# Kernel optimization log

Hardware: AMD Instinct MI355X
Metric: run time of the kernel (lower is better)

The kernel has to match this reference:

```python
import jax, jax.numpy as jnp
import numpy as np

N, E, F_IN, HID, HEADS, OUT_DIM, G = 50000, 600000, 92, 32, 8, 1, 512
EPS = 1e-5


def setup_inputs() -> dict:
    key = jax.random.key(0)
    ks = jax.random.split(key, 30)
    s = 0.1
    d1 = HID * HEADS  # 256
    inp = {
        "x": jax.random.normal(ks[0], (N, F_IN), dtype=jnp.float32),
        "edge_index": jax.random.randint(ks[1], (2, E), 0, N),
        "edge_attr": jax.random.uniform(ks[2], (E, 1), dtype=jnp.float32),
        "batch": jnp.sort(jax.random.randint(ks[3], (N,), 0, G)),
        # conv1 (heads=8, concat)
        "W1": jax.random.normal(ks[4], (F_IN, d1)) * s,
        "We1": jax.random.normal(ks[5], (1, d1)) * s,
        "as1": jax.random.normal(ks[6], (HEADS, HID)) * s,
        "ad1": jax.random.normal(ks[7], (HEADS, HID)) * s,
        "ae1": jax.random.normal(ks[8], (HEADS, HID)) * s,
        "b1": jax.random.normal(ks[9], (d1,)) * s,
        # bn1 (eval mode, running stats)
        "g1": jnp.ones((d1,)), "be1": jnp.zeros((d1,)),
        "m1": jax.random.normal(ks[10], (d1,)) * s, "v1": jnp.ones((d1,)),
        # conv2 (heads=1)
        "W2": jax.random.normal(ks[11], (d1, HID)) * s,
        "We2": jax.random.normal(ks[12], (1, HID)) * s,
        "as2": jax.random.normal(ks[13], (1, HID)) * s,
        "ad2": jax.random.normal(ks[14], (1, HID)) * s,
        "ae2": jax.random.normal(ks[15], (1, HID)) * s,
        "b2": jax.random.normal(ks[16], (HID,)) * s,
        # bn2
        "g2": jnp.ones((HID,)), "be2": jnp.zeros((HID,)),
        "m2": jax.random.normal(ks[17], (HID,)) * s, "v2": jnp.ones((HID,)),
        # final fc
        "fcW": jax.random.normal(ks[18], (HID, OUT_DIM)) * s,
        "fcb": jnp.zeros((OUT_DIM,)),
    }
    return inp


def _gat_conv(x, edge_index, edge_attr, W, We, a_s, a_d, a_e, b, heads, ch):
    """PyG GATConv with edge_dim, add_self_loops=True (fill_value='mean'), concat."""
    n = x.shape[0]
    src, dst = edge_index[0], edge_index[1]
    # self loops: loop edge_attr = mean of incoming edge_attr per node
    cnt = jax.ops.segment_sum(jnp.ones((edge_attr.shape[0],), edge_attr.dtype), dst, n)
    loop_attr = jax.ops.segment_sum(edge_attr, dst, n) / jnp.clip(cnt, 1.0)[:, None]
    ar = jnp.arange(n)
    src = jnp.concatenate([src, ar])
    dst = jnp.concatenate([dst, ar])
    ea = jnp.concatenate([edge_attr, loop_attr], axis=0)
    h = (x @ W).reshape(n, heads, ch)                 # [N,H,C]
    al_s = jnp.sum(h * a_s, axis=-1)                  # [N,H]
    al_d = jnp.sum(h * a_d, axis=-1)                  # [N,H]
    he = (ea @ We).reshape(-1, heads, ch)             # [E',H,C]
    al_e = jnp.sum(he * a_e, axis=-1)                 # [E',H]
    alpha = jax.nn.leaky_relu(al_s[src] + al_d[dst] + al_e, 0.2)
    # scatter softmax over destination segments
    mx = jax.ops.segment_max(alpha, dst, n)
    w = jnp.exp(alpha - mx[dst])
    den = jax.ops.segment_sum(w, dst, n)
    w = w / den[dst]                                  # [E',H]
    out = jax.ops.segment_sum(h[src] * w[:, :, None], dst, n)  # [N,H,C]
    return out.reshape(n, heads * ch) + b


def _bn_eval(x, g, b, m, v):
    return (x - m) * (g / jnp.sqrt(v + EPS)) + b


def reference(x, edge_index, edge_attr, batch,
              W1, We1, as1, ad1, ae1, b1, g1, be1, m1, v1,
              W2, We2, as2, ad2, ae2, b2, g2, be2, m2, v2,
              fcW, fcb):
    h = _gat_conv(x, edge_index, edge_attr, W1, We1, as1, ad1, ae1, b1, HEADS, HID)
    h = jax.nn.relu(_bn_eval(h, g1, be1, m1, v1))
    # dropout is identity in eval mode
    h = _gat_conv(h, edge_index, edge_attr, W2, We2, as2, ad2, ae2, b2, 1, HID)
    h = jax.nn.relu(_bn_eval(h, g2, be2, m2, v2))
    # global mean pool over graphs
    sums = jax.ops.segment_sum(h, batch, G)
    cnt = jax.ops.segment_sum(jnp.ones((h.shape[0],), h.dtype), batch, G)
    pooled = sums / jnp.clip(cnt, 1.0)[:, None]
    return pooled @ fcW + fcb
```

## Files before the change

kernel.cpp:

```cpp
#include <hip/hip_runtime.h>
#include <hip/hip_bf16.h>

#define N_NODES 50000
#define N_EDGES 600000
#define F_IN    92
#define KPAD    96
#define HID     32
#define HEADS   8
#define D1      256
#define HS_LD   264
#define G_GRAPHS 512
#define EPSV    1e-5f
#define NCHUNK  49
#define DEGBLK  2344

using short8  = __attribute__((ext_vector_type(8))) short;
using f32x4   = __attribute__((ext_vector_type(4))) float;
using f32x2   = __attribute__((ext_vector_type(2))) float;

__device__ __forceinline__ float bf2f(unsigned short u) {
    return __uint_as_float(((unsigned)u) << 16);
}
__device__ __forceinline__ unsigned short f2bf(float f) {
    unsigned u = __float_as_uint(f);
    return (unsigned short)((u + 0x7FFFu + ((u >> 16) & 1u)) >> 16);
}


__global__ __launch_bounds__(256) void k_deg_setup(
        const int* __restrict__ ei, int* __restrict__ deg,
        const float* __restrict__ W1, const float* __restrict__ W2,
        const float* __restrict__ We1, const float* __restrict__ ae1,
        const float* __restrict__ We2, const float* __restrict__ ae2,
        const float* __restrict__ as1, const float* __restrict__ ad1,
        const float* __restrict__ b1, const float* __restrict__ g1,
        const float* __restrict__ be1, const float* __restrict__ m1,
        const float* __restrict__ v1,
        const float* __restrict__ b2, const float* __restrict__ g2,
        const float* __restrict__ be2, const float* __restrict__ m2,
        const float* __restrict__ v2,
        unsigned short* __restrict__ W1p, unsigned short* __restrict__ W2p,
        float* __restrict__ va, float* __restrict__ wedot,
        float* __restrict__ bnA1, float* __restrict__ bnB1,
        float* __restrict__ bnA2, float* __restrict__ bnB2) {
    int blk = blockIdx.x, t = threadIdx.x;
    if (blk < DEGBLK) {
        int e = blk * 256 + t;
        if (e < N_EDGES) atomicAdd(&deg[ei[N_EDGES + e]], 1);
        return;
    }
    int b = blk - DEGBLK;
    if (b < 96) {
        int gid = b * 256 + t;
        int k = gid >> 8, col = gid & 255;
        unsigned short v = 0;
        if (k < F_IN) v = f2bf(W1[k * D1 + col]);
        W1p[(((k >> 3) * D1) + col) * 8 + (k & 7)] = v;
    } else if (b < 128) {
        int gid = (b - 96) * 256 + t;
        int k = gid >> 5, col = gid & 31;
        W2p[(((k >> 3) * 32) + col) * 8 + (k & 7)] = f2bf(W2[gid]);
    } else if (b < 134) {
        int gid = (b - 128) * 256 + t;
        if (gid < 2 * HEADS * F_IN) {
            int which = gid / (HEADS * F_IN), rem = gid % (HEADS * F_IN);
            int h = rem / F_IN, k = rem % F_IN;
            const float* av = which ? ad1 : as1;
            float s = 0.f;
            #pragma unroll 8
            for (int c = 0; c < HID; ++c) s += W1[k * D1 + h * HID + c] * av[h * HID + c];
            va[gid] = s;
        }
    } else if (b == 134) {
        if (t < HEADS) {
            float a = 0.f;
            for (int c = 0; c < HID; ++c) a += We1[t * HID + c] * ae1[t * HID + c];
            wedot[t] = a;
        } else if (t == HEADS) {
            float a = 0.f;
            for (int c = 0; c < HID; ++c) a += We2[c] * ae2[c];
            wedot[HEADS] = a;
        }
    } else {
        if (t < D1) {
            float sc = g1[t] * __frsqrt_rn(v1[t] + EPSV);
            bnA1[t] = sc;
            bnB1[t] = (b1[t] - m1[t]) * sc + be1[t];
        }
        if (t < HID) {
            float sc = g2[t] * __frsqrt_rn(v2[t] + EPSV);
            bnA2[t] = sc;
            bnB2[t] = (b2[t] - m2[t]) * sc + be2[t];
        }
    }
}

__global__ void k_partial(const int* __restrict__ deg, int* __restrict__ partials) {
    int b = blockIdx.x;
    int s = 0;
    for (int j = 0; j < 4; ++j) {
        int i = b * 1024 + j * 256 + threadIdx.x;
        if (i < N_NODES) s += deg[i];
    }
    for (int off = 32; off; off >>= 1) s += __shfl_down(s, off, 64);
    __shared__ int sm[4];
    if ((threadIdx.x & 63) == 0) sm[threadIdx.x >> 6] = s;
    __syncthreads();
    if (threadIdx.x == 0) partials[b] = sm[0] + sm[1] + sm[2] + sm[3];
}

__global__ void k_scanc(const int* __restrict__ deg, const int* __restrict__ partials,
                        int* __restrict__ row_off, int* __restrict__ cursor) {
    int b = blockIdx.x;
    int t = threadIdx.x;
    __shared__ int smp;
    if (t < 64) {
        int pv = (t < b) ? partials[t] : 0;
        #pragma unroll
        for (int off = 32; off; off >>= 1) pv += __shfl_down(pv, off, 64);
        if (t == 0) smp = pv;
    }
    int base_i = b * 1024 + t * 4;
    int v[4]; int s = 0;
    #pragma unroll
    for (int j = 0; j < 4; ++j) {
        int i = base_i + j;
        v[j] = (i < N_NODES) ? deg[i] : 0;
        s += v[j];
    }
    __shared__ int sm[256];
    sm[t] = s;
    __syncthreads();
    int val = s;
    for (int off = 1; off < 256; off <<= 1) {
        int add = (t >= off) ? sm[t - off] : 0;
        __syncthreads();
        val += add;
        sm[t] = val;
        __syncthreads();
    }
    int base = smp + (val - s);
    #pragma unroll
    for (int j = 0; j < 4; ++j) {
        int i = base_i + j;
        if (i < N_NODES) { row_off[i] = base; cursor[i] = base; }
        base += v[j];
    }
}

__global__ void k_fill(const int* __restrict__ ei, const float* __restrict__ ea,
                       int* __restrict__ cursor, int2* __restrict__ adj) {
    int e = blockIdx.x * 256 + threadIdx.x;
    if (e < N_EDGES) {
        int d = ei[N_EDGES + e];
        int pos = atomicAdd(&cursor[d], 1);
        adj[pos] = make_int2(ei[e], __float_as_int(ea[e]));
    }
}

__global__ __launch_bounds__(256) void k_conv1(const float* __restrict__ x,
                                               const unsigned short* __restrict__ W1p,
                                               const float* __restrict__ va,
                                               unsigned char* __restrict__ h1f8,
                                               float* __restrict__ al_s,
                                               float* __restrict__ al_d) {
    __shared__ float xs[16 * F_IN];
    __shared__ unsigned short xbs[16 * KPAD];
    __shared__ float hs[16 * HS_LD];
    int n0 = blockIdx.x * 16;
    int t = threadIdx.x;
    for (int i = t; i < 16 * F_IN; i += 256)
        xs[i] = x[(size_t)n0 * F_IN + i];
    __syncthreads();
    for (int i = t; i < 16 * KPAD; i += 256) {
        int r = i / KPAD, k = i - r * KPAD;
        xbs[i] = (k < F_IN) ? f2bf(xs[r * F_IN + k]) : (unsigned short)0;
    }
    {
        int r = t >> 4, j = t & 15;
        const float* vp = va + j * F_IN;
        const float* xr = xs + r * F_IN;
        float s = 0.f;
        for (int k = 0; k < F_IN; ++k) s += xr[k] * vp[k];
        if (j < 8) al_s[(n0 + r) * HEADS + j] = s;
        else       al_d[(n0 + r) * HEADS + (j - 8)] = s;
    }
    __syncthreads();
    int wid = t >> 6, l = t & 63;
    int g = l >> 4, c16 = l & 15;
    const short8* xb = (const short8*)(xbs + c16 * KPAD + g * 8);
    short8 af0 = xb[0], af1 = xb[4], af2 = xb[8];
    const short8* wp = (const short8*)W1p;
    #pragma unroll
    for (int ct = 0; ct < 4; ++ct) {
        int col = (wid * 4 + ct) * 16 + c16;
        f32x4 acc = {0.f, 0.f, 0.f, 0.f};
        acc = __builtin_amdgcn_mfma_f32_16x16x32_bf16(af0, wp[(0 * 4 + g) * D1 + col], acc, 0, 0, 0);
        acc = __builtin_amdgcn_mfma_f32_16x16x32_bf16(af1, wp[(1 * 4 + g) * D1 + col], acc, 0, 0, 0);
        acc = __builtin_amdgcn_mfma_f32_16x16x32_bf16(af2, wp[(2 * 4 + g) * D1 + col], acc, 0, 0, 0);
        #pragma unroll
        for (int r = 0; r < 4; ++r)
            hs[(g * 4 + r) * HS_LD + col] = acc[r];
    }
    __syncthreads();
    {
        int r = t >> 4, q = t & 15;
        #pragma unroll
        for (int j = 0; j < 4; ++j) {
            const float* src = hs + r * HS_LD + q * 4 + j * 64;
            int lo = __builtin_amdgcn_cvt_pk_fp8_f32(src[0], src[1], 0, false);
            int pk = __builtin_amdgcn_cvt_pk_fp8_f32(src[2], src[3], lo, true);
            *(int*)(h1f8 + (size_t)(n0 + r) * D1 + q * 4 + j * 64) = pk;
        }
    }
}

__global__ __launch_bounds__(256) void k_aggr1(
        const int* __restrict__ row_off, const int* __restrict__ deg,
        const int2* __restrict__ adj,
        const unsigned char* __restrict__ h1f8,
        const float* __restrict__ al_s, const float* __restrict__ al_d,
        const float* __restrict__ wedot,
        const float* __restrict__ bnA1, const float* __restrict__ bnB1,
        unsigned short* __restrict__ h1p) {
    int wid = threadIdx.x >> 6, l = threadIdx.x & 63;
    int n = blockIdx.x * 4 + wid;
    if (n >= N_NODES) return;
    int h = l >> 3;
    float wd = wedot[h];
    float dn = al_d[n * HEADS + h];
    int r0 = row_off[n], cnt = deg[n];
    float a0 = 0.f, a1 = 0.f, a2 = 0.f, a3 = 0.f, den = 0.f, ea_sum = 0.f;
    for (int base = 0; base < cnt; base += 64) {
        int m = cnt - base; if (m > 64) m = 64;
        int sl = 0; float el = 0.f;
        if (l < m) {
            int2 se = adj[r0 + base + l];
            sl = se.x;
            el = __int_as_float(se.y);
        }
        for (int i = 0; i < m; ++i) {
            int s = __shfl(sl, i, 64);
            float eav = __shfl(el, i, 64);
            float a = al_s[s * HEADS + h] + dn + eav * wd;
            a = a > 0.f ? a : 0.2f * a;
            float w = __expf(a);
            den += w;
            ea_sum += eav;
            unsigned w8 = *(const unsigned*)(h1f8 + (size_t)s * D1 + l * 4);
            f32x2 lo = __builtin_amdgcn_cvt_pk_f32_fp8(w8, false);
            f32x2 hi = __builtin_amdgcn_cvt_pk_f32_fp8(w8, true);
            a0 += w * lo.x; a1 += w * lo.y;
            a2 += w * hi.x; a3 += w * hi.y;
        }
    }
    {
        float la = ea_sum / (float)(cnt > 0 ? cnt : 1);
        float a = al_s[n * HEADS + h] + dn + la * wd;
        a = a > 0.f ? a : 0.2f * a;
        float w = __expf(a);
        den += w;
        unsigned w8 = *(const unsigned*)(h1f8 + (size_t)n * D1 + l * 4);
        f32x2 lo = __builtin_amdgcn_cvt_pk_f32_fp8(w8, false);
        f32x2 hi = __builtin_amdgcn_cvt_pk_f32_fp8(w8, true);
        a0 += w * lo.x; a1 += w * lo.y;
        a2 += w * hi.x; a3 += w * hi.y;
    }
    float inv = 1.f / den;
    int c = l * 4;
    float4 A = *(const float4*)(bnA1 + c);
    float4 B = *(const float4*)(bnB1 + c);
    ushort4 o;
    o.x = f2bf(fmaxf(a0 * inv * A.x + B.x, 0.f));
    o.y = f2bf(fmaxf(a1 * inv * A.y + B.y, 0.f));
    o.z = f2bf(fmaxf(a2 * inv * A.z + B.z, 0.f));
    o.w = f2bf(fmaxf(a3 * inv * A.w + B.w, 0.f));
    *(ushort4*)(h1p + (size_t)n * D1 + c) = o;
}


__global__ __launch_bounds__(256) void k_gemm2(const unsigned short* __restrict__ h1p,
                                               const unsigned short* __restrict__ W2p,
                                               const float* __restrict__ as2,
                                               const float* __restrict__ ad2,
                                               unsigned char* __restrict__ h2f8,
                                               float* __restrict__ al_s2,
                                               float* __restrict__ al_d2) {
    int wid = threadIdx.x >> 6, l = threadIdx.x & 63;
    int wave = blockIdx.x * 4 + wid;
    if (wave >= N_NODES / 16) return;
    int n0 = wave * 16;
    int g = l >> 4;
    int c16 = l & 15;
    f32x4 acc0 = {0.f, 0.f, 0.f, 0.f};
    f32x4 acc1 = {0.f, 0.f, 0.f, 0.f};
    const short8* ap = (const short8*)(h1p + (size_t)(n0 + c16) * D1 + g * 8);
    const short8* wp = (const short8*)W2p;
    #pragma unroll
    for (int ks = 0; ks < 8; ++ks) {
        short8 afrag = ap[ks * 4];
        short8 b0 = wp[(ks * 4 + g) * 32 + c16];
        short8 b1 = wp[(ks * 4 + g) * 32 + 16 + c16];
        acc0 = __builtin_amdgcn_mfma_f32_16x16x32_bf16(afrag, b0, acc0, 0, 0, 0);
        acc1 = __builtin_amdgcn_mfma_f32_16x16x32_bf16(afrag, b1, acc1, 0, 0, 0);
    }
    float s0 = as2[c16], s1 = as2[16 + c16];
    float d0 = ad2[c16], d1 = ad2[16 + c16];
    float ps[4], pd[4];
    #pragma unroll
    for (int r = 0; r < 4; ++r) {
        int node = n0 + g * 4 + r;
        int p0 = __builtin_amdgcn_cvt_pk_fp8_f32(acc0[r], acc0[r], 0, false);
        int p1 = __builtin_amdgcn_cvt_pk_fp8_f32(acc1[r], acc1[r], 0, false);
        h2f8[(size_t)node * HID + c16]      = (unsigned char)p0;
        h2f8[(size_t)node * HID + 16 + c16] = (unsigned char)p1;
        ps[r] = acc0[r] * s0 + acc1[r] * s1;
        pd[r] = acc0[r] * d0 + acc1[r] * d1;
    }
    #pragma unroll
    for (int off = 1; off < 16; off <<= 1) {
        #pragma unroll
        for (int r = 0; r < 4; ++r) {
            ps[r] += __shfl_xor(ps[r], off, 64);
            pd[r] += __shfl_xor(pd[r], off, 64);
        }
    }
    if (c16 == 0) {
        #pragma unroll
        for (int r = 0; r < 4; ++r) {
            int node = n0 + g * 4 + r;
            al_s2[node] = ps[r];
            al_d2[node] = pd[r];
        }
    }
}

__global__ __launch_bounds__(256) void k_aggr2(
        const int* __restrict__ row_off, const int* __restrict__ deg,
        const int2* __restrict__ adj,
        const unsigned char* __restrict__ h2f8,
        const float* __restrict__ al_s2, const float* __restrict__ al_d2,
        const float* __restrict__ wedot,
        const float* __restrict__ bnA2, const float* __restrict__ bnB2,
        float* __restrict__ h2p) {
    int wid = threadIdx.x >> 6, l = threadIdx.x & 63;
    int n = blockIdx.x * 4 + wid;
    if (n >= N_NODES) return;
    int g = l >> 3, c8 = l & 7;
    float wd = wedot[HEADS];
    float dn = al_d2[n];
    int r0 = row_off[n], cnt = deg[n];
    float a0 = 0.f, a1 = 0.f, a2 = 0.f, a3 = 0.f, den = 0.f, ea_sum = 0.f;
    for (int base = 0; base < cnt; base += 64) {
        int m = cnt - base; if (m > 64) m = 64;
        int sl = 0; float el = 0.f;
        if (l < m) {
            int2 se = adj[r0 + base + l];
            sl = se.x;
            el = __int_as_float(se.y);
        }
        for (int i = 0; i < m; i += 8) {
            int j = i + g;
            int jj = j < m ? j : 0;
            int s = __shfl(sl, jj, 64);
            float eav = __shfl(el, jj, 64);
            if (j < m) {
                float a = al_s2[s] + dn + eav * wd;
                a = a > 0.f ? a : 0.2f * a;
                float w = __expf(a);
                den += w;
                ea_sum += eav;
                unsigned w8 = *(const unsigned*)(h2f8 + (size_t)s * HID + c8 * 4);
                f32x2 lo = __builtin_amdgcn_cvt_pk_f32_fp8(w8, false);
                f32x2 hi = __builtin_amdgcn_cvt_pk_f32_fp8(w8, true);
                a0 += w * lo.x; a1 += w * lo.y;
                a2 += w * hi.x; a3 += w * hi.y;
            }
        }
    }
    #pragma unroll
    for (int off = 8; off < 64; off <<= 1) {
        a0 += __shfl_xor(a0, off, 64);
        a1 += __shfl_xor(a1, off, 64);
        a2 += __shfl_xor(a2, off, 64);
        a3 += __shfl_xor(a3, off, 64);
        den += __shfl_xor(den, off, 64);
        ea_sum += __shfl_xor(ea_sum, off, 64);
    }
    {
        float la = ea_sum / (float)(cnt > 0 ? cnt : 1);
        float a = al_s2[n] + dn + la * wd;
        a = a > 0.f ? a : 0.2f * a;
        float w = __expf(a);
        den += w;
        unsigned w8 = *(const unsigned*)(h2f8 + (size_t)n * HID + c8 * 4);
        f32x2 lo = __builtin_amdgcn_cvt_pk_f32_fp8(w8, false);
        f32x2 hi = __builtin_amdgcn_cvt_pk_f32_fp8(w8, true);
        a0 += w * lo.x; a1 += w * lo.y;
        a2 += w * hi.x; a3 += w * hi.y;
    }
    if (g == 0) {
        float inv = 1.f / den;
        int c = c8 * 4;
        float4 A = *(const float4*)(bnA2 + c);
        float4 B = *(const float4*)(bnB2 + c);
        float4 y;
        y.x = fmaxf(a0 * inv * A.x + B.x, 0.f);
        y.y = fmaxf(a1 * inv * A.y + B.y, 0.f);
        y.z = fmaxf(a2 * inv * A.z + B.z, 0.f);
        y.w = fmaxf(a3 * inv * A.w + B.w, 0.f);
        *(float4*)(h2p + (size_t)n * HID + c) = y;
    }
}

__global__ __launch_bounds__(64) void k_poolfc(const float* __restrict__ h2p,
                                               const int* __restrict__ batch,
                                               const float* __restrict__ fcW,
                                               const float* __restrict__ fcb,
                                               float* __restrict__ out) {
    int g = blockIdx.x;
    int l = threadIdx.x;
    auto lb = [&](int key) {
        int lo = 0, hi = N_NODES;
        while (lo < hi) {
            int mid = (lo + hi) >> 1;
            if (batch[mid] < key) lo = mid + 1; else hi = mid;
        }
        return lo;
    };
    int s0 = lb(g), s1 = lb(g + 1);
    int c = l & 31, half = l >> 5;
    float acc = 0.f;
    for (int r = s0 + half; r < s1; r += 2)
        acc += h2p[(size_t)r * HID + c];
    acc += __shfl_xor(acc, 32, 64);
    int cn = s1 - s0;
    float mean = acc / (float)(cn > 0 ? cn : 1);
    float p = mean * fcW[c];
    #pragma unroll
    for (int off = 1; off < 32; off <<= 1) p += __shfl_xor(p, off, 64);
    if (l == 0) out[g] = p + fcb[0];
}


extern "C" void kernel_launch(void* const* d_in, const int* in_sizes, int n_in,
                              void* d_out, int out_size, void* d_ws, size_t ws_size,
                              hipStream_t stream) {
    const float* x    = (const float*)d_in[0];
    const int*   ei   = (const int*)  d_in[1];
    const float* ea   = (const float*)d_in[2];
    const int*   batch= (const int*)  d_in[3];
    const float* W1   = (const float*)d_in[4];
    const float* We1  = (const float*)d_in[5];
    const float* as1  = (const float*)d_in[6];
    const float* ad1  = (const float*)d_in[7];
    const float* ae1  = (const float*)d_in[8];
    const float* b1   = (const float*)d_in[9];
    const float* g1   = (const float*)d_in[10];
    const float* be1  = (const float*)d_in[11];
    const float* m1   = (const float*)d_in[12];
    const float* v1   = (const float*)d_in[13];
    const float* W2   = (const float*)d_in[14];
    const float* We2  = (const float*)d_in[15];
    const float* as2  = (const float*)d_in[16];
    const float* ad2  = (const float*)d_in[17];
    const float* ae2  = (const float*)d_in[18];
    const float* b2   = (const float*)d_in[19];
    const float* g2   = (const float*)d_in[20];
    const float* be2  = (const float*)d_in[21];
    const float* m2   = (const float*)d_in[22];
    const float* v2   = (const float*)d_in[23];
    const float* fcW  = (const float*)d_in[24];
    const float* fcb  = (const float*)d_in[25];
    float* out = (float*)d_out;

    char* ws = (char*)d_ws;
    size_t off = 0;
    auto alloc = [&](size_t bytes) -> void* {
        void* p = ws + off;
        off += (bytes + 255) & ~(size_t)255;
        return p;
    };
    int*   deg     = (int*)  alloc((size_t)N_NODES * 4);
    int*   row_off = (int*)  alloc((size_t)N_NODES * 4);
    int*   cursor  = (int*)  alloc((size_t)N_NODES * 4);
    int2*  adj     = (int2*) alloc((size_t)N_EDGES * 8);
    float* al_s1   = (float*)alloc((size_t)N_NODES * HEADS * 4);
    float* al_d1   = (float*)alloc((size_t)N_NODES * HEADS * 4);
    float* al_s2   = (float*)alloc((size_t)N_NODES * 4);
    float* al_d2   = (float*)alloc((size_t)N_NODES * 4);
    float* wedot   = (float*)alloc(16 * 4);
    float* va      = (float*)alloc((size_t)2 * HEADS * F_IN * 4);
    int*   partials= (int*)  alloc(64 * 4);
    float* bnA1    = (float*)alloc((size_t)D1 * 4);
    float* bnB1    = (float*)alloc((size_t)D1 * 4);
    float* bnA2    = (float*)alloc((size_t)HID * 4);
    float* bnB2    = (float*)alloc((size_t)HID * 4);
    unsigned short* W1p = (unsigned short*)alloc((size_t)KPAD * D1 * 2);
    unsigned short* W2p = (unsigned short*)alloc((size_t)D1 * HID * 2);
    unsigned char*  h1f8 = (unsigned char*)alloc((size_t)N_NODES * D1);
    unsigned short* h1p = (unsigned short*)alloc((size_t)N_NODES * D1 * 2);
    unsigned char*  h2f8 = (unsigned char*)alloc((size_t)N_NODES * HID);
    float* h2p     = (float*)alloc((size_t)N_NODES * HID * 4);
    (void)ws_size; (void)in_sizes; (void)n_in; (void)out_size;

    hipMemsetAsync(deg, 0, (size_t)N_NODES * 4, stream);

    k_deg_setup<<<DEGBLK + 136, 256, 0, stream>>>(ei, deg, W1, W2, We1, ae1, We2, ae2,
                                                  as1, ad1, b1, g1, be1, m1, v1,
                                                  b2, g2, be2, m2, v2,
                                                  W1p, W2p, va, wedot,
                                                  bnA1, bnB1, bnA2, bnB2);
    k_partial<<<NCHUNK, 256, 0, stream>>>(deg, partials);
    k_scanc<<<NCHUNK, 256, 0, stream>>>(deg, partials, row_off, cursor);
    k_fill<<<(N_EDGES + 255) / 256, 256, 0, stream>>>(ei, ea, cursor, adj);

    k_conv1<<<N_NODES / 16, 256, 0, stream>>>(x, W1p, va, h1f8, al_s1, al_d1);
    k_aggr1<<<(N_NODES + 3) / 4, 256, 0, stream>>>(row_off, deg, adj,
                                                   h1f8, al_s1, al_d1, wedot,
                                                   bnA1, bnB1, h1p);

    k_gemm2<<<(N_NODES / 16 + 3) / 4, 256, 0, stream>>>(h1p, W2p, as2, ad2, h2f8, al_s2, al_d2);
    k_aggr2<<<(N_NODES + 3) / 4, 256, 0, stream>>>(row_off, deg, adj,
                                                   h2f8, al_s2, al_d2, wedot, bnA2, bnB2, h2p);
    k_poolfc<<<G_GRAPHS, 64, 0, stream>>>(h2p, batch, fcW, fcb, out);
}
```

Measured before the change: 214.3 us.

## Merge scan kernels, replace memset with zero kernel, batch gathers in aggr1

The degree zeroing moves from hipMemsetAsync to a small vectorized kernel. The two-pass prefix scan becomes one kernel in which each block recomputes its own prefix by summing all preceding degrees. The conv1 aggregation inner loop is unrolled by 8 so that the neighbor attention scalars and fp8 feature words are gathered together before use, which gives more loads in flight to hide gather latency. The trade-offs are redundant prefix reads in later scan blocks and higher register pressure in aggr1.

Measured after the change: 229.1 us. +6.9%, slower.

```diff
diff --git a/kernel.cpp b/kernel.cpp
--- a/kernel.cpp
+++ b/kernel.cpp
@@ -24,6 +24,14 @@
 __device__ __forceinline__ unsigned short f2bf(float f) {
     unsigned u = __float_as_uint(f);
     return (unsigned short)((u + 0x7FFFu + ((u >> 16) & 1u)) >> 16);
+}
+
+__global__ void k_zero(int* __restrict__ deg) {
+    int i = blockIdx.x * 256 + threadIdx.x;
+    if (i < N_NODES / 4) {
+        int4 z = {0, 0, 0, 0};
+        *(int4*)(deg + i * 4) = z;
+    }
 }
 
 
@@ -95,40 +103,32 @@
     }
 }
 
-__global__ void k_partial(const int* __restrict__ deg, int* __restrict__ partials) {
-    int b = blockIdx.x;
-    int s = 0;
-    for (int j = 0; j < 4; ++j) {
-        int i = b * 1024 + j * 256 + threadIdx.x;
-        if (i < N_NODES) s += deg[i];
-    }
-    for (int off = 32; off; off >>= 1) s += __shfl_down(s, off, 64);
-    __shared__ int sm[4];
-    if ((threadIdx.x & 63) == 0) sm[threadIdx.x >> 6] = s;
-    __syncthreads();
-    if (threadIdx.x == 0) partials[b] = sm[0] + sm[1] + sm[2] + sm[3];
-}
-
-__global__ void k_scanc(const int* __restrict__ deg, const int* __restrict__ partials,
-                        int* __restrict__ row_off, int* __restrict__ cursor) {
+__global__ __launch_bounds__(256) void k_scan1(const int* __restrict__ deg,
+                                               int* __restrict__ row_off,
+                                               int* __restrict__ cursor) {
     int b = blockIdx.x;
     int t = threadIdx.x;
+    __shared__ int sm[256];
     __shared__ int smp;
+    int p = 0;
+    for (int i = t; i < b * 1024; i += 256) p += deg[i];
+    sm[t] = p;
+    __syncthreads();
     if (t < 64) {
-        int pv = (t < b) ? partials[t] : 0;
+        int v = sm[t] + sm[t + 64] + sm[t + 128] + sm[t + 192];
         #pragma unroll
-        for (int off = 32; off; off >>= 1) pv += __shfl_down(pv, off, 64);
-        if (t == 0) smp = pv;
-    }
+        for (int off = 32; off; off >>= 1) v += __shfl_down(v, off, 64);
+        if (t == 0) smp = v;
+    }
+    __syncthreads();
     int base_i = b * 1024 + t * 4;
-    int v[4]; int s = 0;
+    int v4[4]; int s = 0;
     #pragma unroll
     for (int j = 0; j < 4; ++j) {
         int i = base_i + j;
-        v[j] = (i < N_NODES) ? deg[i] : 0;
-        s += v[j];
-    }
-    __shared__ int sm[256];
+        v4[j] = (i < N_NODES) ? deg[i] : 0;
+        s += v4[j];
+    }
     sm[t] = s;
     __syncthreads();
     int val = s;
@@ -144,7 +144,7 @@
     for (int j = 0; j < 4; ++j) {
         int i = base_i + j;
         if (i < N_NODES) { row_off[i] = base; cursor[i] = base; }
-        base += v[j];
+        base += v4[j];
     }
 }
 
@@ -239,7 +239,33 @@
             sl = se.x;
             el = __int_as_float(se.y);
         }
-        for (int i = 0; i < m; ++i) {
+        int i = 0;
+        for (; i + 7 < m; i += 8) {
+            int sv[8]; float ev[8], asv[8]; unsigned wv[8];
+            #pragma unroll
+            for (int j = 0; j < 8; ++j) {
+                sv[j] = __shfl(sl, i + j, 64);
+                ev[j] = __shfl(el, i + j, 64);
+            }
+            #pragma unroll
+            for (int j = 0; j < 8; ++j) asv[j] = al_s[sv[j] * HEADS + h];
+            #pragma unroll
+            for (int j = 0; j < 8; ++j)
+                wv[j] = *(const unsigned*)(h1f8 + (size_t)sv[j] * D1 + l * 4);
+            #pragma unroll
+            for (int j = 0; j < 8; ++j) {
+                float aa = asv[j] + dn + ev[j] * wd;
+                aa = aa > 0.f ? aa : 0.2f * aa;
+                float w = __expf(aa);
+                den += w;
+                ea_sum += ev[j];
+                f32x2 lo = __builtin_amdgcn_cvt_pk_f32_fp8(wv[j], false);
+                f32x2 hi = __builtin_amdgcn_cvt_pk_f32_fp8(wv[j], true);
+                a0 += w * lo.x; a1 += w * lo.y;
+                a2 += w * hi.x; a3 += w * hi.y;
+            }
+        }
+        for (; i < m; ++i) {
             int s = __shfl(sl, i, 64);
             float eav = __shfl(el, i, 64);
             float a = al_s[s * HEADS + h] + dn + eav * wd;
@@ -491,7 +517,6 @@
     float* al_d2   = (float*)alloc((size_t)N_NODES * 4);
     float* wedot   = (float*)alloc(16 * 4);
     float* va      = (float*)alloc((size_t)2 * HEADS * F_IN * 4);
-    int*   partials= (int*)  alloc(64 * 4);
     float* bnA1    = (float*)alloc((size_t)D1 * 4);
     float* bnB1    = (float*)alloc((size_t)D1 * 4);
     float* bnA2    = (float*)alloc((size_t)HID * 4);
@@ -504,15 +529,13 @@
     float* h2p     = (float*)alloc((size_t)N_NODES * HID * 4);
     (void)ws_size; (void)in_sizes; (void)n_in; (void)out_size;
 
-    hipMemsetAsync(deg, 0, (size_t)N_NODES * 4, stream);
-
+    k_zero<<<(N_NODES / 4 + 255) / 256, 256, 0, stream>>>(deg);
     k_deg_setup<<<DEGBLK + 136, 256, 0, stream>>>(ei, deg, W1, W2, We1, ae1, We2, ae2,
                                                   as1, ad1, b1, g1, be1, m1, v1,
                                                   b2, g2, be2, m2, v2,
                                                   W1p, W2p, va, wedot,
                                                   bnA1, bnB1, bnA2, bnB2);
-    k_partial<<<NCHUNK, 256, 0, stream>>>(deg, partials);
-    k_scanc<<<NCHUNK, 256, 0, stream>>>(deg, partials, row_off, cursor);
+    k_scan1<<<NCHUNK, 256, 0, stream>>>(deg, row_off, cursor);
     k_fill<<<(N_EDGES + 255) / 256, 256, 0, stream>>>(ei, ea, cursor, adj);
 
     k_conv1<<<N_NODES / 16, 256, 0, stream>>>(x, W1p, va, h1f8, al_s1, al_d1);
```
